# Kernel tuning notes

Measured on AMD Instinct MI355X. Metric: run time of the kernel, lower is better.

Reference implementation:

```python
import jax, jax.numpy as jnp
import numpy as np

B, S, D_MODEL, H = 2, 2048, 1024, 16
HD = D_MODEL // H  # 64
THETA = 10000.0


def setup_inputs() -> dict:
    key = jax.random.key(0)
    ks = jax.random.split(key, 5)
    std = (2.0 / (D_MODEL + D_MODEL)) ** 0.5
    x = jax.random.normal(ks[0], (B, S, D_MODEL), dtype=jnp.float32)
    Wq = jax.random.normal(ks[1], (D_MODEL, D_MODEL), dtype=jnp.float32) * std
    Wk = jax.random.normal(ks[2], (D_MODEL, D_MODEL), dtype=jnp.float32) * std
    Wv = jax.random.normal(ks[3], (D_MODEL, D_MODEL), dtype=jnp.float32) * std
    Wo = jax.random.normal(ks[4], (D_MODEL, D_MODEL), dtype=jnp.float32) * std
    # RoPE tables (buffers)
    pos = jnp.arange(S, dtype=jnp.float32)
    freq = THETA ** (-jnp.arange(0, HD, 2, dtype=jnp.float32) / HD)  # [HD/2]
    ang = jnp.outer(pos, freq)  # [S, HD/2]
    token_positions = jnp.arange(S, dtype=jnp.int32)
    return {
        "x": x,
        "token_positions": token_positions,
        "use_rope": 1,
        "Wq": Wq, "Wk": Wk, "Wv": Wv, "Wo": Wo,
        "cos": jnp.cos(ang), "sin": jnp.sin(ang),
    }


def _apply_rope(t, c, sn):
    # t: [b,h,s,d]; c,sn: [s,d/2] (broadcast over b,h)
    e = t[..., 0::2]
    o = t[..., 1::2]
    return jnp.stack([e * c - o * sn, o * c + e * sn], axis=-1).reshape(t.shape)


def reference(x, token_positions, use_rope, Wq, Wk, Wv, Wo, cos, sin):
    b, s, _ = x.shape

    def split_heads(t):  # [b,s,D] -> [b,h,s,hd]
        return t.reshape(b, s, H, HD).transpose(0, 2, 1, 3)

    q = split_heads(x @ Wq.T)
    k = split_heads(x @ Wk.T)
    v = split_heads(x @ Wv.T)

    if use_rope:
        c = cos[token_positions]   # [s, hd/2]
        sn = sin[token_positions]  # [s, hd/2]
        q = _apply_rope(q, c, sn)
        k = _apply_rope(k, c, sn)

    scale = 1.0 / jnp.sqrt(jnp.float32(HD))
    scores = jnp.einsum('bhqd,bhkd->bhqk', q, k) * scale  # [b,h,s,s]
    causal = jnp.tril(jnp.ones((s, s), dtype=bool))
    scores = jnp.where(causal, scores, -jnp.inf)
    attn = jax.nn.softmax(scores, axis=-1)
    y = jnp.einsum('bhqk,bhkd->bhqd', attn, v)
    y = y.transpose(0, 2, 1, 3).reshape(b, s, D_MODEL)
    return y @ Wo.T
```

## Files before the change

kernel.cpp:

```cpp
#include <hip/hip_runtime.h>
#include <math.h>

#define BB 2
#define SS 2048
#define DM 1024
#define NH 16
#define HD 64

typedef __attribute__((ext_vector_type(8))) __bf16 bf16x8;
typedef __attribute__((ext_vector_type(4))) __bf16 bf16x4;
typedef __attribute__((ext_vector_type(8))) unsigned short u16x8;
typedef __attribute__((ext_vector_type(4))) float f32x4;
typedef unsigned short u16;
typedef unsigned int u32;
typedef __attribute__((address_space(1))) unsigned int u32g;
typedef __attribute__((address_space(3))) unsigned int u32l;

#define CEXP 0.18033688011112042f

static __device__ __forceinline__ u16 f2bf(float f) {
    __bf16 h = (__bf16)f;
    return __builtin_bit_cast(unsigned short, h);
}

static __device__ __forceinline__ void gld16(const u16* g, u16* l) {
    __builtin_amdgcn_global_load_lds((const u32g*)g, (u32l*)l, 16, 0, 0);
}

__global__ __launch_bounds__(256)
void cast_all(const float* __restrict__ x,
              const float* __restrict__ wq, const float* __restrict__ wk,
              const float* __restrict__ wv, const float* __restrict__ wo,
              u16* __restrict__ xb, u16* __restrict__ wqb, u16* __restrict__ wkb,
              u16* __restrict__ wvb, u16* __restrict__ wob)
{
    const int N4X = (BB * SS * DM) / 4;
    const int N4W = (DM * DM) / 4;
    int i = blockIdx.x * 256 + threadIdx.x;
    const float* src; u16* dst; int off;
    if (i < N4X) { src = x; dst = xb; off = i; }
    else {
        int i2 = i - N4X;
        int w = i2 >> 18;
        off = i2 & (N4W - 1);
        switch (w) {
            case 0:  src = wq; dst = wqb; break;
            case 1:  src = wk; dst = wkb; break;
            case 2:  src = wv; dst = wvb; break;
            default: src = wo; dst = wob; break;
        }
    }
    float4 v = ((const float4*)src)[off];
    ushort4 o;
    o.x = f2bf(v.x); o.y = f2bf(v.y); o.z = f2bf(v.z); o.w = f2bf(v.w);
    ((ushort4*)dst)[off] = o;
}

__global__ __launch_bounds__(256, 3)
void qkv_gemm(const u16* __restrict__ X,
              const u16* __restrict__ Wq, const u16* __restrict__ Wk,
              const u16* __restrict__ Wv,
              const int* __restrict__ tp, const float* __restrict__ cosp,
              const float* __restrict__ sinp, const int* __restrict__ use_rope,
              u16* __restrict__ Q, u16* __restrict__ K, u16* __restrict__ V)
{
    const u16* W; u16* dst;
    if (blockIdx.z == 0)      { W = Wq; dst = Q; }
    else if (blockIdx.z == 1) { W = Wk; dst = K; }
    else                      { W = Wv; dst = V; }

    __shared__ u16 SH[4 * 64 * 68];
    u16* As = SH;
    u16* Bs = SH + 8192;
    const int t  = threadIdx.x;
    const int wv = t >> 6, L = t & 63, ln = L & 15, qd = L >> 4;
    const int i0 = blockIdx.y * 128, j0 = blockIdx.x * 128;
    const int wm = (wv >> 1) * 64, wn = (wv & 1) * 64;
    const int srow = L >> 3;
    const int scg  = ((L & 7) ^ (L >> 3)) * 8;

    f32x4 acc[4][4];
    #pragma unroll
    for (int a = 0; a < 4; ++a)
        #pragma unroll
        for (int b = 0; b < 4; ++b)
            #pragma unroll
            for (int e = 0; e < 4; ++e) acc[a][b][e] = 0.f;

    for (int k0 = 0; k0 < DM; k0 += 64) {
        __syncthreads();
        #pragma unroll
        for (int g = 0; g < 4; ++g) {
            int rb = wv * 32 + g * 8;
            gld16(X + (size_t)(i0 + rb + srow) * DM + k0 + scg, &As[rb * 64]);
            gld16(W + (size_t)(j0 + rb + srow) * DM + k0 + scg, &Bs[rb * 64]);
        }
        __syncthreads();
        bf16x8 a[4][2], b[4][2];
        #pragma unroll
        for (int mi = 0; mi < 4; ++mi)
            #pragma unroll
            for (int kd = 0; kd < 2; ++kd)
                a[mi][kd] = *(const bf16x8*)&As[(wm + mi * 16 + ln) * 64 + (((kd * 4 + qd) ^ (ln & 7)) * 8)];
        #pragma unroll
        for (int ni = 0; ni < 4; ++ni)
            #pragma unroll
            for (int kd = 0; kd < 2; ++kd)
                b[ni][kd] = *(const bf16x8*)&Bs[(wn + ni * 16 + ln) * 64 + (((kd * 4 + qd) ^ (ln & 7)) * 8)];
        #pragma unroll
        for (int kd = 0; kd < 2; ++kd)
            #pragma unroll
            for (int mi = 0; mi < 4; ++mi)
                #pragma unroll
                for (int ni = 0; ni < 4; ++ni)
                    acc[mi][ni] = __builtin_amdgcn_mfma_f32_16x16x32_bf16(a[mi][kd], b[ni][kd], acc[mi][ni], 0, 0, 0);
    }

    const int rope_on = (blockIdx.z < 2) ? use_rope[0] : 0;
    if (rope_on) {
        #pragma unroll
        for (int mi = 0; mi < 4; ++mi)
            #pragma unroll
            for (int r = 0; r < 4; ++r) {
                int gi = i0 + wm + mi * 16 + qd * 4 + r;
                int s = gi & 2047;
                int pos = tp[s];
                #pragma unroll
                for (int ni = 0; ni < 4; ++ni) {
                    int d = wn + ni * 16 + ln;
                    int dh = d & 63;
                    float c  = cosp[pos * 32 + (dh >> 1)];
                    float sn = sinp[pos * 32 + (dh >> 1)];
                    float v = acc[mi][ni][r];
                    float pv = __shfl_xor(v, 1);
                    acc[mi][ni][r] = (dh & 1) ? (v * c + pv * sn) : (v * c - pv * sn);
                }
            }
    }

    __syncthreads();
    u16* Ts = SH + wv * (64 * 68);
    #pragma unroll
    for (int mi = 0; mi < 4; ++mi)
        #pragma unroll
        for (int ni = 0; ni < 4; ++ni)
            #pragma unroll
            for (int r = 0; r < 4; ++r)
                Ts[(mi * 16 + qd * 4 + r) * 68 + ni * 16 + ln] = f2bf(acc[mi][ni][r]);

    const int h  = blockIdx.x * 2 + (wv & 1);
    const int sb = i0 + wm;
    const int b_ = sb >> 11, s0 = sb & 2047;
    if (blockIdx.z < 2) {
        const int lrow = L >> 3, lcol = (L & 7) * 8;
        #pragma unroll
        for (int r2 = 0; r2 < 8; ++r2) {
            int row = lrow + r2 * 8;
            u16x8 val = *(const u16x8*)&Ts[row * 68 + lcol];
            *(u16x8*)&dst[(((size_t)(b_ * NH + h)) * SS + s0 + row) * HD + lcol] = val;
        }
    } else {
        const int sch = (L & 7) * 8;
        const int dr0 = L >> 3;
        #pragma unroll
        for (int r2 = 0; r2 < 8; ++r2) {
            int d = dr0 + r2 * 8;
            u16x8 val;
            #pragma unroll
            for (int u = 0; u < 8; ++u) val[u] = Ts[(sch + u) * 68 + d];
            *(u16x8*)&dst[(((size_t)(b_ * NH + h)) * HD + d) * SS + s0 + sch] = val;
        }
    }
}

__global__ __launch_bounds__(256, 2)
void out_gemm(const u16* __restrict__ X, const u16* __restrict__ W,
              float* __restrict__ dst)
{
    __shared__ char SHB[36864];
    u16* As = (u16*)SHB;
    u16* Bs = (u16*)SHB + 8192;
    const int t  = threadIdx.x;
    const int wv = t >> 6, L = t & 63, ln = L & 15, qd = L >> 4;
    const int i0 = blockIdx.y * 128, j0 = blockIdx.x * 64;
    const int wm = (wv >> 1) * 64, wn = (wv & 1) * 32;
    const int srow = L >> 3;
    const int scg  = ((L & 7) ^ (L >> 3)) * 8;

    f32x4 acc[4][2];
    #pragma unroll
    for (int mi = 0; mi < 4; ++mi)
        #pragma unroll
        for (int ni = 0; ni < 2; ++ni)
            #pragma unroll
            for (int e = 0; e < 4; ++e) acc[mi][ni][e] = 0.f;

    for (int k0 = 0; k0 < DM; k0 += 64) {
        __syncthreads();
        #pragma unroll
        for (int g = 0; g < 4; ++g) {
            int rb = wv * 32 + g * 8;
            gld16(X + (size_t)(i0 + rb + srow) * DM + k0 + scg, &As[rb * 64]);
        }
        #pragma unroll
        for (int g = 0; g < 2; ++g) {
            int rb = wv * 16 + g * 8;
            gld16(W + (size_t)(j0 + rb + srow) * DM + k0 + scg, &Bs[rb * 64]);
        }
        __syncthreads();
        bf16x8 a[4][2], b[2][2];
        #pragma unroll
        for (int mi = 0; mi < 4; ++mi)
            #pragma unroll
            for (int kd = 0; kd < 2; ++kd)
                a[mi][kd] = *(const bf16x8*)&As[(wm + mi * 16 + ln) * 64 + (((kd * 4 + qd) ^ (ln & 7)) * 8)];
        #pragma unroll
        for (int ni = 0; ni < 2; ++ni)
            #pragma unroll
            for (int kd = 0; kd < 2; ++kd)
                b[ni][kd] = *(const bf16x8*)&Bs[(wn + ni * 16 + ln) * 64 + (((kd * 4 + qd) ^ (ln & 7)) * 8)];
        #pragma unroll
        for (int kd = 0; kd < 2; ++kd)
            #pragma unroll
            for (int mi = 0; mi < 4; ++mi)
                #pragma unroll
                for (int ni = 0; ni < 2; ++ni)
                    acc[mi][ni] = __builtin_amdgcn_mfma_f32_16x16x32_bf16(a[mi][kd], b[ni][kd], acc[mi][ni], 0, 0, 0);
    }

    __syncthreads();
    float* Ts = (float*)SHB + wv * (64 * 36);
    #pragma unroll
    for (int mi = 0; mi < 4; ++mi)
        #pragma unroll
        for (int ni = 0; ni < 2; ++ni)
            #pragma unroll
            for (int r = 0; r < 4; ++r)
                Ts[(mi * 16 + qd * 4 + r) * 36 + ni * 16 + ln] = acc[mi][ni][r];

    const int lrow = L >> 3, lch = L & 7;
    #pragma unroll
    for (int r2 = 0; r2 < 8; ++r2) {
        int row = lrow + r2 * 8;
        float4 v = *(const float4*)&Ts[row * 36 + lch * 4];
        *(float4*)&dst[(size_t)(i0 + wm + row) * DM + j0 + wn + lch * 4] = v;
    }
}

static __device__ __forceinline__ void group_step(
    const u16* KsB, const bf16x8 qf[2], u16* psw,
    bool diag, int rowg, int j0, int ln, int qd,
    float& m, float& l, f32x4* o, bf16x8& pf0, bf16x8& pf1)
{
    const int pm = 2 * (ln & 7);
    f32x4 s[4];
    #pragma unroll
    for (int mt = 0; mt < 4; ++mt) {
        bf16x8 a0 = *(const bf16x8*)&KsB[(mt * 16 + ln) * 64 + ((qd ^ (ln & 7)) * 8)];
        bf16x8 a1 = *(const bf16x8*)&KsB[(mt * 16 + ln) * 64 + (((4 + qd) ^ (ln & 7)) * 8)];
        #pragma unroll
        for (int e = 0; e < 4; ++e) s[mt][e] = 0.f;
        s[mt] = __builtin_amdgcn_mfma_f32_16x16x32_bf16(a0, qf[0], s[mt], 0, 0, 0);
        s[mt] = __builtin_amdgcn_mfma_f32_16x16x32_bf16(a1, qf[1], s[mt], 0, 0, 0);
    }
    if (diag) {
        #pragma unroll
        for (int mt = 0; mt < 4; ++mt)
            #pragma unroll
            for (int r = 0; r < 4; ++r)
                if (j0 + mt * 16 + qd * 4 + r > rowg) s[mt][r] = -3.0e38f;
    }
    float rm = s[0][0];
    #pragma unroll
    for (int mt = 0; mt < 4; ++mt)
        #pragma unroll
        for (int r = 0; r < 4; ++r) rm = fmaxf(rm, s[mt][r]);
    rm = fmaxf(rm, __shfl_xor(rm, 16));
    rm = fmaxf(rm, __shfl_xor(rm, 32));
    float nm = fmaxf(m, rm);
    float alpha = exp2f((m - nm) * CEXP);
    float nmc = nm * CEXP;
    float rs = 0.f;
    #pragma unroll
    for (int mt = 0; mt < 4; ++mt) {
        bf16x4 pk;
        #pragma unroll
        for (int r = 0; r < 4; ++r) {
            float pv = exp2f(fmaf(s[mt][r], CEXP, -nmc));
            rs += pv;
            pk[r] = (__bf16)pv;
        }
        *(bf16x4*)(psw + ln * 64 + ((mt * 4 + qd) ^ pm) * 4) = pk;
    }
    rs += __shfl_xor(rs, 16);
    rs += __shfl_xor(rs, 32);
    l = l * alpha + rs;
    m = nm;
    #pragma unroll
    for (int ni = 0; ni < 4; ++ni)
        #pragma unroll
        for (int r = 0; r < 4; ++r) o[ni][r] *= alpha;
    pf0 = *(const bf16x8*)(psw + ln * 64 + ((qd * 2) ^ pm) * 4);
    pf1 = *(const bf16x8*)(psw + ln * 64 + ((8 + qd * 2) ^ pm) * 4);
}

__global__ __launch_bounds__(512, 2)
void attn_kernel(const u16* __restrict__ Q, const u16* __restrict__ K,
                 const u16* __restrict__ V, u16* __restrict__ Y)
{
    __shared__ u16 Ks[2][2][64 * 64];
    __shared__ u16 Vt[2][2][64 * 64];
    __shared__ u16 Ps[8][16 * 64];

    const int t  = threadIdx.x;
    const int wv = t >> 6, L = t & 63, ln = L & 15, qd = L >> 4;
    const int grp = wv >> 2, wsub = wv & 3;
    const int bh = blockIdx.x, p = blockIdx.y;
    const u16* Qp = Q + (size_t)bh * SS * HD;
    const u16* Kp = K + (size_t)bh * SS * HD;
    const u16* Vp = V + (size_t)bh * HD * SS;
    const int srow = L >> 3;
    const int scg  = ((L & 7) ^ (L >> 3)) * 8;
    const int b = bh >> 4, h = bh & 15;

    float* MB = (float*)&Ks[1][0][0];
    float* ML = (float*)&Ps[4][0];

    #pragma unroll 1
    for (int ph = 0; ph < 2; ++ph) {
        const int qt    = ph ? (31 - p) : p;
        const int qb    = qt * 64;
        const int ntile = qt + 1;
        const int half0 = ntile >> 1;
        const int I     = ntile - half0;
        const int base  = grp ? half0 : 0;
        const int cnt   = grp ? I : half0;

        bf16x8 qf[2];
        {
            const u16* rq = Qp + (size_t)(qb + wsub * 16 + ln) * HD;
            qf[0] = *(const bf16x8*)(rq + qd * 8);
            qf[1] = *(const bf16x8*)(rq + 32 + qd * 8);
        }

        f32x4 o[4];
        #pragma unroll
        for (int ni = 0; ni < 4; ++ni)
            #pragma unroll
            for (int e = 0; e < 4; ++e) o[ni][e] = 0.f;
        float m = -3.0e38f, l = 0.f;

        if (cnt > 0) {
            #pragma unroll
            for (int g = 0; g < 2; ++g) {
                int rb = wsub * 16 + g * 8;
                gld16(Kp + (size_t)(base * 64 + rb + srow) * HD + scg, &Ks[grp][0][rb * 64]);
                gld16(Vp + (size_t)(rb + srow) * SS + base * 64 + scg, &Vt[grp][0][rb * 64]);
            }
        }
        __syncthreads();

        #pragma unroll 1
        for (int tix = 0; tix < I; ++tix) {
            const int buf = tix & 1;

            if (tix + 1 < cnt) {
                const int j1 = (base + tix + 1) * 64;
                #pragma unroll
                for (int g = 0; g < 2; ++g) {
                    int rb = wsub * 16 + g * 8;
                    gld16(Kp + (size_t)(j1 + rb + srow) * HD + scg, &Ks[grp][buf ^ 1][rb * 64]);
                    gld16(Vp + (size_t)(rb + srow) * SS + j1 + scg, &Vt[grp][buf ^ 1][rb * 64]);
                }
            }

            if (tix < cnt) {
                const int gt = base + tix;
                bf16x8 pf0, pf1;
                group_step(&Ks[grp][buf][0], qf, &Ps[wv][0],
                           grp && (tix == cnt - 1),
                           qb + wsub * 16 + ln, gt * 64, ln, qd, m, l, o, pf0, pf1);
                #pragma unroll
                for (int kc = 0; kc < 2; ++kc)
                    #pragma unroll
                    for (int ni = 0; ni < 4; ++ni) {
                        bf16x8 vf = *(const bf16x8*)&Vt[grp][buf][(ni * 16 + ln) * 64 + (((kc * 4 + qd) ^ (ln & 7)) * 8)];
                        o[ni] = __builtin_amdgcn_mfma_f32_16x16x32_bf16(vf, kc ? pf1 : pf0, o[ni], 0, 0, 0);
                    }
            }
            __syncthreads();
        }

        const int writer = ph ? 0 : 1;
        const int q = wsub * 16 + ln;
        if (grp == writer) {
            if (qd == 0) { ML[q] = m; ML[64 + q] = l; }
            #pragma unroll
            for (int ni = 0; ni < 4; ++ni)
                *(f32x4*)&MB[q * 64 + ni * 16 + qd * 4] = o[ni];
        }
        __syncthreads();
        if (grp != writer) {
            float mp = ML[q], lp = ML[64 + q];
            float mf = fmaxf(m, mp);
            float as = exp2f((m - mf) * CEXP);
            float ap = exp2f((mp - mf) * CEXP);
            float lf = as * l + ap * lp;
            float inv = 1.f / lf;
            const int sq = qb + q;
            #pragma unroll
            for (int ni = 0; ni < 4; ++ni) {
                f32x4 op = *(const f32x4*)&MB[q * 64 + ni * 16 + qd * 4];
                bf16x4 pk;
                #pragma unroll
                for (int r = 0; r < 4; ++r)
                    pk[r] = (__bf16)((as * o[ni][r] + ap * op[r]) * inv);
                *(bf16x4*)&Y[((size_t)(b * SS + sq)) * DM + h * HD + ni * 16 + qd * 4] = pk;
            }
        }
        __syncthreads();
    }
}

extern "C" void kernel_launch(void* const* d_in, const int* in_sizes, int n_in,
                              void* d_out, int out_size, void* d_ws, size_t ws_size,
                              hipStream_t stream)
{
    const float* x        = (const float*)d_in[0];
    const int*   tp       = (const int*)d_in[1];
    const int*   use_rope = (const int*)d_in[2];
    const float* Wq       = (const float*)d_in[3];
    const float* Wk       = (const float*)d_in[4];
    const float* Wv       = (const float*)d_in[5];
    const float* Wo       = (const float*)d_in[6];
    const float* cosp     = (const float*)d_in[7];
    const float* sinp     = (const float*)d_in[8];
    float* out = (float*)d_out;

    char* ws = (char*)d_ws;
    const size_t MB = 1 << 20;
    u16* xb  = (u16*)(ws);
    u16* Wqb = (u16*)(ws + 8 * MB);
    u16* Wkb = (u16*)(ws + 10 * MB);
    u16* Wvb = (u16*)(ws + 12 * MB);
    u16* Wob = (u16*)(ws + 14 * MB);
    u16* Qb  = (u16*)(ws + 16 * MB);
    u16* Kb  = (u16*)(ws + 24 * MB);
    u16* Vb  = (u16*)(ws + 32 * MB);
    u16* Yb  = (u16*)(ws + 40 * MB);

    cast_all<<<8192, 256, 0, stream>>>(x, Wq, Wk, Wv, Wo, xb, Wqb, Wkb, Wvb, Wob);
    qkv_gemm<<<dim3(DM / 128, BB * SS / 128, 3), 256, 0, stream>>>(
        xb, Wqb, Wkb, Wvb, tp, cosp, sinp, use_rope, Qb, Kb, Vb);
    attn_kernel<<<dim3(BB * NH, 16), 512, 0, stream>>>(Qb, Kb, Vb, Yb);
    out_gemm<<<dim3(DM / 64, BB * SS / 128), 256, 0, stream>>>(Yb, Wob, out);
}
```

Before: 186.6 us.

## Add lazy softmax rescaling, prefetch V fragments, swizzle merge buffer, raise occupancy

The flash-attention step now computes exponentials against the running max and only rescales the accumulator and l when some lane's new max exceeds the old one by more than a threshold (FA4-style lazy rescale). This removes the rescale multiplies in most iterations, at the cost of recomputing the exponentials when the branch is taken. The first half of the V fragments is also loaded from LDS before the QK step so the loads overlap with it. The merge buffer gets an XOR swizzle to avoid LDS bank conflicts, and launch bounds now ask for 4 blocks per CU, which limits registers and risks spills.

Result: no change. 186.9 us (+0.1%).

```diff
diff --git a/kernel.cpp b/kernel.cpp
--- a/kernel.cpp
+++ b/kernel.cpp
@@ -270,6 +270,15 @@
             for (int r = 0; r < 4; ++r)
                 if (j0 + mt * 16 + qd * 4 + r > rowg) s[mt][r] = -3.0e38f;
     }
+
+    float p[16];
+    float nmc = m * CEXP;
+    #pragma unroll
+    for (int mt = 0; mt < 4; ++mt)
+        #pragma unroll
+        for (int r = 0; r < 4; ++r)
+            p[mt * 4 + r] = exp2f(fmaf(s[mt][r], CEXP, -nmc));
+
     float rm = s[0][0];
     #pragma unroll
     for (int mt = 0; mt < 4; ++mt)
@@ -277,34 +286,43 @@
         for (int r = 0; r < 4; ++r) rm = fmaxf(rm, s[mt][r]);
     rm = fmaxf(rm, __shfl_xor(rm, 16));
     rm = fmaxf(rm, __shfl_xor(rm, 32));
-    float nm = fmaxf(m, rm);
-    float alpha = exp2f((m - nm) * CEXP);
-    float nmc = nm * CEXP;
+
+    if (__any((rm - m) * CEXP > 8.0f)) {
+        float nm = fmaxf(m, rm);
+        float alpha = exp2f((m - nm) * CEXP);
+        nmc = nm * CEXP;
+        #pragma unroll
+        for (int mt = 0; mt < 4; ++mt)
+            #pragma unroll
+            for (int r = 0; r < 4; ++r)
+                p[mt * 4 + r] = exp2f(fmaf(s[mt][r], CEXP, -nmc));
+        #pragma unroll
+        for (int ni = 0; ni < 4; ++ni)
+            #pragma unroll
+            for (int r = 0; r < 4; ++r) o[ni][r] *= alpha;
+        l *= alpha;
+        m = nm;
+    }
+
     float rs = 0.f;
     #pragma unroll
     for (int mt = 0; mt < 4; ++mt) {
         bf16x4 pk;
         #pragma unroll
         for (int r = 0; r < 4; ++r) {
-            float pv = exp2f(fmaf(s[mt][r], CEXP, -nmc));
-            rs += pv;
-            pk[r] = (__bf16)pv;
+            rs += p[mt * 4 + r];
+            pk[r] = (__bf16)p[mt * 4 + r];
         }
         *(bf16x4*)(psw + ln * 64 + ((mt * 4 + qd) ^ pm) * 4) = pk;
     }
     rs += __shfl_xor(rs, 16);
     rs += __shfl_xor(rs, 32);
-    l = l * alpha + rs;
-    m = nm;
-    #pragma unroll
-    for (int ni = 0; ni < 4; ++ni)
-        #pragma unroll
-        for (int r = 0; r < 4; ++r) o[ni][r] *= alpha;
+    l += rs;
     pf0 = *(const bf16x8*)(psw + ln * 64 + ((qd * 2) ^ pm) * 4);
     pf1 = *(const bf16x8*)(psw + ln * 64 + ((8 + qd * 2) ^ pm) * 4);
 }
 
-__global__ __launch_bounds__(512, 2)
+__global__ __launch_bounds__(512, 4)
 void attn_kernel(const u16* __restrict__ Q, const u16* __restrict__ K,
                  const u16* __restrict__ V, u16* __restrict__ Y)
 {
@@ -376,17 +394,22 @@
 
             if (tix < cnt) {
                 const int gt = base + tix;
+                bf16x8 vf0[4];
+                #pragma unroll
+                for (int ni = 0; ni < 4; ++ni)
+                    vf0[ni] = *(const bf16x8*)&Vt[grp][buf][(ni * 16 + ln) * 64 + ((qd ^ (ln & 7)) * 8)];
                 bf16x8 pf0, pf1;
                 group_step(&Ks[grp][buf][0], qf, &Ps[wv][0],
                            grp && (tix == cnt - 1),
                            qb + wsub * 16 + ln, gt * 64, ln, qd, m, l, o, pf0, pf1);
                 #pragma unroll
-                for (int kc = 0; kc < 2; ++kc)
-                    #pragma unroll
-                    for (int ni = 0; ni < 4; ++ni) {
-                        bf16x8 vf = *(const bf16x8*)&Vt[grp][buf][(ni * 16 + ln) * 64 + (((kc * 4 + qd) ^ (ln & 7)) * 8)];
-                        o[ni] = __builtin_amdgcn_mfma_f32_16x16x32_bf16(vf, kc ? pf1 : pf0, o[ni], 0, 0, 0);
-                    }
+                for (int ni = 0; ni < 4; ++ni)
+                    o[ni] = __builtin_amdgcn_mfma_f32_16x16x32_bf16(vf0[ni], pf0, o[ni], 0, 0, 0);
+                #pragma unroll
+                for (int ni = 0; ni < 4; ++ni) {
+                    bf16x8 vf = *(const bf16x8*)&Vt[grp][buf][(ni * 16 + ln) * 64 + (((4 + qd) ^ (ln & 7)) * 8)];
+                    o[ni] = __builtin_amdgcn_mfma_f32_16x16x32_bf16(vf, pf1, o[ni], 0, 0, 0);
+                }
             }
             __syncthreads();
         }
@@ -397,7 +420,7 @@
             if (qd == 0) { ML[q] = m; ML[64 + q] = l; }
             #pragma unroll
             for (int ni = 0; ni < 4; ++ni)
-                *(f32x4*)&MB[q * 64 + ni * 16 + qd * 4] = o[ni];
+                *(f32x4*)&MB[q * 64 + (((ni * 4 + qd) ^ (q & 15)) * 4)] = o[ni];
         }
         __syncthreads();
         if (grp != writer) {
@@ -410,7 +433,7 @@
             const int sq = qb + q;
             #pragma unroll
             for (int ni = 0; ni < 4; ++ni) {
-                f32x4 op = *(const f32x4*)&MB[q * 64 + ni * 16 + qd * 4];
+                f32x4 op = *(const f32x4*)&MB[q * 64 + (((ni * 4 + qd) ^ (q & 15)) * 4)];
                 bf16x4 pk;
                 #pragma unroll
                 for (int r = 0; r < 4; ++r)
```
